# Performance work log

Measured on AMD Instinct MI355X. Metric: run time of the kernel, lower is better.

The kernel has to match this reference:

```python
import jax, jax.numpy as jnp
import numpy as np


def setup_inputs() -> dict:
    key = jax.random.key(0)
    k1, k2 = jax.random.split(key)
    N, M, D = 2048, 2048, 64
    z_x = jax.random.normal(k1, (N, D), dtype=jnp.float32)
    z_y = jax.random.normal(k2, (M, D), dtype=jnp.float32)
    return {"z_x": z_x, "z_y": z_y}


def reference(z_x, z_y):
    # s[i, j] = -sum_d |z_x[i, d] - z_y[j, d]|  -> [N, M]
    s = -jnp.sum(jnp.abs(z_x[:, None, :] - z_y[None, :, :]), axis=-1)
    a = jax.nn.softmax(s, axis=1)  # row softmax
    b = jax.nn.softmax(s, axis=0)  # column softmax
    w = a + b - a * b              # soft-or combination of alignments
    c = jnp.sum(w * s) / jnp.sum(w)
    return c
```

## Files before the change

kernel.cpp:

```cpp
#include <hip/hip_runtime.h>

#define NROWS 2048
#define MCOLS 2048
#define DDIM  64
#define TILE  64
#define NTI   32
#define NTJ   32

__device__ __forceinline__ void stage_tiles(
    const float* __restrict__ zx, const float* __restrict__ zy,
    int bi, int bj, float (*sX)[TILE], float (*sY)[TILE])
{
  int t = threadIdx.x;
  int r  = t & 63;
  int d0 = (t >> 6) << 2;
  const float* zxp = zx + (size_t)(bi * TILE + r) * DDIM;
  const float* zyp = zy + (size_t)(bj * TILE + r) * DDIM;
#pragma unroll
  for (int q = 0; q < 4; ++q) {
    int d = d0 + 16 * q;
    float4 xv = *(const float4*)(zxp + d);
    float4 yv = *(const float4*)(zyp + d);
    sX[d+0][r]=xv.x; sX[d+1][r]=xv.y; sX[d+2][r]=xv.z; sX[d+3][r]=xv.w;
    sY[d+0][r]=yv.x; sY[d+1][r]=yv.y; sY[d+2][r]=yv.z; sY[d+3][r]=yv.w;
  }
}

__device__ __forceinline__ void compute_sv(
    const float (*sX)[TILE], const float (*sY)[TILE],
    int i0, int j0, float sv[4][4])
{
  float acc[4][4] = {{0.f}};
#pragma unroll 8
  for (int d = 0; d < DDIM; ++d) {
    float4 xv = *(const float4*)&sX[d][i0];
    float4 yv = *(const float4*)&sY[d][j0];
    float xr[4] = {xv.x, xv.y, xv.z, xv.w};
    float yc[4] = {yv.x, yv.y, yv.z, yv.w};
#pragma unroll
    for (int a = 0; a < 4; ++a)
#pragma unroll
      for (int b = 0; b < 4; ++b)
        acc[a][b] += fabsf(xr[a] - yc[b]);
  }
#pragma unroll
  for (int a = 0; a < 4; ++a)
#pragma unroll
    for (int b = 0; b < 4; ++b)
      sv[a][b] = -acc[a][b];
}

__global__ __launch_bounds__(256) void k1_dist(
    const float* __restrict__ zx, const float* __restrict__ zy,
    float* __restrict__ s_out,
    float* __restrict__ rm_part, float* __restrict__ rs_part,
    float* __restrict__ cm_part, float* __restrict__ cs_part)
{
  __shared__ float sX[DDIM][TILE];
  __shared__ float sY[DDIM][TILE];
  __shared__ float cmw[4][TILE];
  __shared__ float csw[4][TILE];

  int bi = blockIdx.y, bj = blockIdx.x;
  int t  = threadIdx.x;
  int lid = t & 63, wv = t >> 6;
  int i0 = (t >> 4) << 2, j0 = (t & 15) << 2;

  stage_tiles(zx, zy, bi, bj, sX, sY);
  __syncthreads();
  float sv[4][4];
  compute_sv(sX, sY, i0, j0, sv);

#pragma unroll
  for (int a = 0; a < 4; ++a) {
    float4 v = make_float4(sv[a][0], sv[a][1], sv[a][2], sv[a][3]);
    *(float4*)(s_out + (size_t)(bi * TILE + i0 + a) * MCOLS + bj * TILE + j0) = v;
  }

  float rm[4], es[4];
#pragma unroll
  for (int a = 0; a < 4; ++a)
    rm[a] = fmaxf(fmaxf(sv[a][0], sv[a][1]), fmaxf(sv[a][2], sv[a][3]));
#pragma unroll
  for (int off = 1; off <= 8; off <<= 1)
#pragma unroll
    for (int a = 0; a < 4; ++a)
      rm[a] = fmaxf(rm[a], __shfl_xor(rm[a], off));
#pragma unroll
  for (int a = 0; a < 4; ++a)
    es[a] = __expf(sv[a][0]-rm[a]) + __expf(sv[a][1]-rm[a])
          + __expf(sv[a][2]-rm[a]) + __expf(sv[a][3]-rm[a]);
#pragma unroll
  for (int off = 1; off <= 8; off <<= 1)
#pragma unroll
    for (int a = 0; a < 4; ++a)
      es[a] += __shfl_xor(es[a], off);
  if ((lid & 15) == 0) {
#pragma unroll
    for (int a = 0; a < 4; ++a) {
      int idx = bj * NROWS + bi * TILE + i0 + a;
      rm_part[idx] = rm[a];
      rs_part[idx] = es[a];
    }
  }

  float cm[4], ce[4];
#pragma unroll
  for (int b = 0; b < 4; ++b)
    cm[b] = fmaxf(fmaxf(sv[0][b], sv[1][b]), fmaxf(sv[2][b], sv[3][b]));
#pragma unroll
  for (int off = 16; off <= 32; off <<= 1)
#pragma unroll
    for (int b = 0; b < 4; ++b)
      cm[b] = fmaxf(cm[b], __shfl_xor(cm[b], off));
#pragma unroll
  for (int b = 0; b < 4; ++b)
    ce[b] = __expf(sv[0][b]-cm[b]) + __expf(sv[1][b]-cm[b])
          + __expf(sv[2][b]-cm[b]) + __expf(sv[3][b]-cm[b]);
#pragma unroll
  for (int off = 16; off <= 32; off <<= 1)
#pragma unroll
    for (int b = 0; b < 4; ++b)
      ce[b] += __shfl_xor(ce[b], off);
  if (lid < 16) {
#pragma unroll
    for (int b = 0; b < 4; ++b) {
      cmw[wv][lid * 4 + b] = cm[b];
      csw[wv][lid * 4 + b] = ce[b];
    }
  }
  __syncthreads();
  if (t < TILE) {
    int j = t;
    float M = fmaxf(fmaxf(cmw[0][j], cmw[1][j]), fmaxf(cmw[2][j], cmw[3][j]));
    float S = __expf(cmw[0][j]-M)*csw[0][j] + __expf(cmw[1][j]-M)*csw[1][j]
            + __expf(cmw[2][j]-M)*csw[2][j] + __expf(cmw[3][j]-M)*csw[3][j];
    int idx = bi * MCOLS + bj * TILE + j;
    cm_part[idx] = M;
    cs_part[idx] = S;
  }
}

__global__ __launch_bounds__(256) void k2_combine(
    const float* __restrict__ s_in,
    const float* __restrict__ rm_part, const float* __restrict__ rs_part,
    const float* __restrict__ cm_part, const float* __restrict__ cs_part,
    float* __restrict__ part )
{
  __shared__ float l_rmax[TILE], l_rinv[TILE];
  __shared__ float l_cmax[TILE], l_cinv[TILE];
  __shared__ float red[8];

  int bi = blockIdx.y, bj = blockIdx.x;
  int t  = threadIdx.x;
  int lid = t & 63, wv = t >> 6;
  int i0 = (t >> 4) << 2, j0 = (t & 15) << 2;

  if (t < 64) {
    int i = bi * TILE + t;
    float m[NTJ];
#pragma unroll
    for (int tj = 0; tj < NTJ; ++tj) m[tj] = rm_part[tj * NROWS + i];
    float M = m[0];
#pragma unroll
    for (int tj = 1; tj < NTJ; ++tj) M = fmaxf(M, m[tj]);
    float S = 0.f;
#pragma unroll
    for (int tj = 0; tj < NTJ; ++tj)
      S += __expf(m[tj] - M) * rs_part[tj * NROWS + i];
    l_rmax[t] = M;
    l_rinv[t] = 1.f / S;
  } else if (t < 128) {
    int c = t - 64;
    int j = bj * TILE + c;
    float m[NTI];
#pragma unroll
    for (int ti = 0; ti < NTI; ++ti) m[ti] = cm_part[ti * MCOLS + j];
    float M = m[0];
#pragma unroll
    for (int ti = 1; ti < NTI; ++ti) M = fmaxf(M, m[ti]);
    float S = 0.f;
#pragma unroll
    for (int ti = 0; ti < NTI; ++ti)
      S += __expf(m[ti] - M) * cs_part[ti * MCOLS + j];
    l_cmax[c] = M;
    l_cinv[c] = 1.f / S;
  }
  __syncthreads();

  float sv[4][4];
  {
    const float* base = s_in + (size_t)(bi * TILE + i0) * MCOLS + bj * TILE + j0;
#pragma unroll
    for (int a = 0; a < 4; ++a) {
      float4 v = *(const float4*)(base + (size_t)a * MCOLS);
      sv[a][0] = v.x; sv[a][1] = v.y; sv[a][2] = v.z; sv[a][3] = v.w;
    }
  }
  float rm[4], rv[4], cm[4], cv[4];
#pragma unroll
  for (int a = 0; a < 4; ++a) {
    rm[a] = l_rmax[i0 + a];
    rv[a] = l_rinv[i0 + a];
  }
#pragma unroll
  for (int b = 0; b < 4; ++b) {
    cm[b] = l_cmax[j0 + b];
    cv[b] = l_cinv[j0 + b];
  }
  float pn = 0.f, pd = 0.f;
#pragma unroll
  for (int a = 0; a < 4; ++a)
#pragma unroll
    for (int b = 0; b < 4; ++b) {
      float av = __expf(sv[a][b] - rm[a]) * rv[a];
      float bv = __expf(sv[a][b] - cm[b]) * cv[b];
      float w  = av + bv - av * bv;
      pn += w * sv[a][b];
      pd += w;
    }
#pragma unroll
  for (int off = 1; off <= 32; off <<= 1) {
    pn += __shfl_xor(pn, off);
    pd += __shfl_xor(pd, off);
  }
  if (lid == 0) { red[wv * 2] = pn; red[wv * 2 + 1] = pd; }
  __syncthreads();
  if (t == 0) {
    int bid = bi * NTJ + bj;
    part[bid * 2 + 0] = red[0] + red[2] + red[4] + red[6];
    part[bid * 2 + 1] = red[1] + red[3] + red[5] + red[7];
  }
}

__global__ __launch_bounds__(256) void k3_out(
    const float* __restrict__ part, float* __restrict__ out)
{
  int t = threadIdx.x;
  float pn = 0.f, pd = 0.f;
#pragma unroll
  for (int k = t; k < NTI * NTJ; k += 256) {
    float2 v = *(const float2*)(part + k * 2);
    pn += v.x;
    pd += v.y;
  }
#pragma unroll
  for (int off = 1; off <= 32; off <<= 1) {
    pn += __shfl_xor(pn, off);
    pd += __shfl_xor(pd, off);
  }
  __shared__ float red[8];
  if ((t & 63) == 0) { red[(t >> 6) * 2] = pn; red[(t >> 6) * 2 + 1] = pd; }
  __syncthreads();
  if (t == 0) {
    float n = red[0] + red[2] + red[4] + red[6];
    float d = red[1] + red[3] + red[5] + red[7];
    out[0] = n / d;
  }
}

extern "C" void kernel_launch(void* const* d_in, const int* in_sizes, int n_in,
                              void* d_out, int out_size, void* d_ws, size_t ws_size,
                              hipStream_t stream)
{
  const float* zx = (const float*)d_in[0];
  const float* zy = (const float*)d_in[1];
  float* out = (float*)d_out;

  char* ws = (char*)d_ws;
  float* part    = (float*)(ws + 0);
  float* rm_part = (float*)(ws + (64  << 10));
  float* rs_part = (float*)(ws + (320 << 10));
  float* cm_part = (float*)(ws + (576 << 10));
  float* cs_part = (float*)(ws + (832 << 10));
  float* s_buf   = (float*)(ws + (1088 << 10));

  dim3 grid(NTJ, NTI), block(256);
  k1_dist   <<<grid, block, 0, stream>>>(zx, zy, s_buf,
                                         rm_part, rs_part, cm_part, cs_part);
  k2_combine<<<grid, block, 0, stream>>>(s_buf,
                                         rm_part, rs_part, cm_part, cs_part, part);
  k3_out    <<<dim3(1), block, 0, stream>>>(part, out);
}
```

Baseline: 35.71 us.

## Enlarge distance tile to 128x64 with 8x4 per-thread microtile and nontemporal S traffic

```diff
diff --git a/kernel.cpp b/kernel.cpp
--- a/kernel.cpp
+++ b/kernel.cpp
@@ -3,52 +3,14 @@
 #define NROWS 2048
 #define MCOLS 2048
 #define DDIM  64
-#define TILE  64
-#define NTI   32
-#define NTJ   32
-
-__device__ __forceinline__ void stage_tiles(
-    const float* __restrict__ zx, const float* __restrict__ zy,
-    int bi, int bj, float (*sX)[TILE], float (*sY)[TILE])
-{
-  int t = threadIdx.x;
-  int r  = t & 63;
-  int d0 = (t >> 6) << 2;
-  const float* zxp = zx + (size_t)(bi * TILE + r) * DDIM;
-  const float* zyp = zy + (size_t)(bj * TILE + r) * DDIM;
-#pragma unroll
-  for (int q = 0; q < 4; ++q) {
-    int d = d0 + 16 * q;
-    float4 xv = *(const float4*)(zxp + d);
-    float4 yv = *(const float4*)(zyp + d);
-    sX[d+0][r]=xv.x; sX[d+1][r]=xv.y; sX[d+2][r]=xv.z; sX[d+3][r]=xv.w;
-    sY[d+0][r]=yv.x; sY[d+1][r]=yv.y; sY[d+2][r]=yv.z; sY[d+3][r]=yv.w;
-  }
-}
-
-__device__ __forceinline__ void compute_sv(
-    const float (*sX)[TILE], const float (*sY)[TILE],
-    int i0, int j0, float sv[4][4])
-{
-  float acc[4][4] = {{0.f}};
-#pragma unroll 8
-  for (int d = 0; d < DDIM; ++d) {
-    float4 xv = *(const float4*)&sX[d][i0];
-    float4 yv = *(const float4*)&sY[d][j0];
-    float xr[4] = {xv.x, xv.y, xv.z, xv.w};
-    float yc[4] = {yv.x, yv.y, yv.z, yv.w};
-#pragma unroll
-    for (int a = 0; a < 4; ++a)
-#pragma unroll
-      for (int b = 0; b < 4; ++b)
-        acc[a][b] += fabsf(xr[a] - yc[b]);
-  }
-#pragma unroll
-  for (int a = 0; a < 4; ++a)
-#pragma unroll
-    for (int b = 0; b < 4; ++b)
-      sv[a][b] = -acc[a][b];
-}
+#define TI    128
+#define TJ    64
+#define NTI1  (NROWS / TI)
+#define NTJ   (MCOLS / TJ)
+#define TILE2 64
+#define NTI2  (NROWS / TILE2)
+
+typedef float f32x4 __attribute__((ext_vector_type(4)));
 
 __global__ __launch_bounds__(256) void k1_dist(
     const float* __restrict__ zx, const float* __restrict__ zy,
@@ -56,88 +18,139 @@
     float* __restrict__ rm_part, float* __restrict__ rs_part,
     float* __restrict__ cm_part, float* __restrict__ cs_part)
 {
-  __shared__ float sX[DDIM][TILE];
-  __shared__ float sY[DDIM][TILE];
-  __shared__ float cmw[4][TILE];
-  __shared__ float csw[4][TILE];
-
-  int bi = blockIdx.y, bj = blockIdx.x;
-  int t  = threadIdx.x;
-  int lid = t & 63, wv = t >> 6;
-  int i0 = (t >> 4) << 2, j0 = (t & 15) << 2;
-
-  stage_tiles(zx, zy, bi, bj, sX, sY);
-  __syncthreads();
-  float sv[4][4];
-  compute_sv(sX, sY, i0, j0, sv);
-
-#pragma unroll
-  for (int a = 0; a < 4; ++a) {
-    float4 v = make_float4(sv[a][0], sv[a][1], sv[a][2], sv[a][3]);
-    *(float4*)(s_out + (size_t)(bi * TILE + i0 + a) * MCOLS + bj * TILE + j0) = v;
-  }
-
-  float rm[4], es[4];
-#pragma unroll
-  for (int a = 0; a < 4; ++a)
-    rm[a] = fmaxf(fmaxf(sv[a][0], sv[a][1]), fmaxf(sv[a][2], sv[a][3]));
-#pragma unroll
-  for (int off = 1; off <= 8; off <<= 1)
-#pragma unroll
-    for (int a = 0; a < 4; ++a)
-      rm[a] = fmaxf(rm[a], __shfl_xor(rm[a], off));
-#pragma unroll
-  for (int a = 0; a < 4; ++a)
-    es[a] = __expf(sv[a][0]-rm[a]) + __expf(sv[a][1]-rm[a])
-          + __expf(sv[a][2]-rm[a]) + __expf(sv[a][3]-rm[a]);
-#pragma unroll
-  for (int off = 1; off <= 8; off <<= 1)
-#pragma unroll
-    for (int a = 0; a < 4; ++a)
-      es[a] += __shfl_xor(es[a], off);
-  if ((lid & 15) == 0) {
-#pragma unroll
-    for (int a = 0; a < 4; ++a) {
-      int idx = bj * NROWS + bi * TILE + i0 + a;
-      rm_part[idx] = rm[a];
-      rs_part[idx] = es[a];
-    }
-  }
-
-  float cm[4], ce[4];
-#pragma unroll
-  for (int b = 0; b < 4; ++b)
-    cm[b] = fmaxf(fmaxf(sv[0][b], sv[1][b]), fmaxf(sv[2][b], sv[3][b]));
-#pragma unroll
-  for (int off = 16; off <= 32; off <<= 1)
+  __shared__ float sX[DDIM][TI];
+  __shared__ float sY[DDIM][TJ];
+  __shared__ float cmw[4][TJ];
+  __shared__ float csw[4][TJ];
+
+  const int bi = blockIdx.y, bj = blockIdx.x;
+  const int t  = threadIdx.x;
+  const int lid = t & 63, wv = t >> 6;
+  const int i0 = (t >> 4) << 3;
+  const int j0 = (t & 15) << 2;
+
+  {
+    int r = t & 127, half = t >> 7;
+    const float* zxp = zx + (size_t)(bi * TI + r) * DDIM + half * 32;
+#pragma unroll
+    for (int q = 0; q < 8; ++q) {
+      float4 v = *(const float4*)(zxp + q * 4);
+      int d = half * 32 + q * 4;
+      sX[d+0][r]=v.x; sX[d+1][r]=v.y; sX[d+2][r]=v.z; sX[d+3][r]=v.w;
+    }
+  }
+  {
+    int r = t & 63, quad = t >> 6;
+    const float* zyp = zy + (size_t)(bj * TJ + r) * DDIM + quad * 16;
+#pragma unroll
+    for (int q = 0; q < 4; ++q) {
+      float4 v = *(const float4*)(zyp + q * 4);
+      int d = quad * 16 + q * 4;
+      sY[d+0][r]=v.x; sY[d+1][r]=v.y; sY[d+2][r]=v.z; sY[d+3][r]=v.w;
+    }
+  }
+  __syncthreads();
+
+  float acc[8][4] = {{0.f}};
+#pragma unroll 4
+  for (int d = 0; d < DDIM; ++d) {
+    float4 x0 = *(const float4*)&sX[d][i0];
+    float4 x1 = *(const float4*)&sX[d][i0 + 4];
+    float4 yv = *(const float4*)&sY[d][j0];
+    float xr[8] = {x0.x, x0.y, x0.z, x0.w, x1.x, x1.y, x1.z, x1.w};
+    float yc[4] = {yv.x, yv.y, yv.z, yv.w};
+#pragma unroll
+    for (int a = 0; a < 8; ++a)
+#pragma unroll
+      for (int b = 0; b < 4; ++b)
+        acc[a][b] += fabsf(xr[a] - yc[b]);
+  }
+  float sv[8][4];
+#pragma unroll
+  for (int a = 0; a < 8; ++a)
 #pragma unroll
     for (int b = 0; b < 4; ++b)
-      cm[b] = fmaxf(cm[b], __shfl_xor(cm[b], off));
-#pragma unroll
-  for (int b = 0; b < 4; ++b)
-    ce[b] = __expf(sv[0][b]-cm[b]) + __expf(sv[1][b]-cm[b])
-          + __expf(sv[2][b]-cm[b]) + __expf(sv[3][b]-cm[b]);
-#pragma unroll
-  for (int off = 16; off <= 32; off <<= 1)
-#pragma unroll
-    for (int b = 0; b < 4; ++b)
-      ce[b] += __shfl_xor(ce[b], off);
-  if (lid < 16) {
+      sv[a][b] = -acc[a][b];
+
+#pragma unroll
+  for (int a = 0; a < 8; ++a) {
+    f32x4 v = { sv[a][0], sv[a][1], sv[a][2], sv[a][3] };
+    __builtin_nontemporal_store(v,
+        (f32x4*)(s_out + (size_t)(bi * TI + i0 + a) * MCOLS + bj * TJ + j0));
+  }
+
+  {
+    float rm[8], es[8];
+#pragma unroll
+    for (int a = 0; a < 8; ++a)
+      rm[a] = fmaxf(fmaxf(sv[a][0], sv[a][1]), fmaxf(sv[a][2], sv[a][3]));
+#pragma unroll
+    for (int off = 1; off <= 8; off <<= 1)
+#pragma unroll
+      for (int a = 0; a < 8; ++a)
+        rm[a] = fmaxf(rm[a], __shfl_xor(rm[a], off));
+#pragma unroll
+    for (int a = 0; a < 8; ++a)
+      es[a] = __expf(sv[a][0]-rm[a]) + __expf(sv[a][1]-rm[a])
+            + __expf(sv[a][2]-rm[a]) + __expf(sv[a][3]-rm[a]);
+#pragma unroll
+    for (int off = 1; off <= 8; off <<= 1)
+#pragma unroll
+      for (int a = 0; a < 8; ++a)
+        es[a] += __shfl_xor(es[a], off);
+    if ((lid & 15) == 0) {
+#pragma unroll
+      for (int a = 0; a < 8; ++a) {
+        int idx = bj * NROWS + bi * TI + i0 + a;
+        rm_part[idx] = rm[a];
+        rs_part[idx] = es[a];
+      }
+    }
+  }
+
+  {
+    float cm[4], ce[4];
 #pragma unroll
     for (int b = 0; b < 4; ++b) {
-      cmw[wv][lid * 4 + b] = cm[b];
-      csw[wv][lid * 4 + b] = ce[b];
-    }
-  }
-  __syncthreads();
-  if (t < TILE) {
-    int j = t;
-    float M = fmaxf(fmaxf(cmw[0][j], cmw[1][j]), fmaxf(cmw[2][j], cmw[3][j]));
-    float S = __expf(cmw[0][j]-M)*csw[0][j] + __expf(cmw[1][j]-M)*csw[1][j]
-            + __expf(cmw[2][j]-M)*csw[2][j] + __expf(cmw[3][j]-M)*csw[3][j];
-    int idx = bi * MCOLS + bj * TILE + j;
-    cm_part[idx] = M;
-    cs_part[idx] = S;
+      float m = sv[0][b];
+#pragma unroll
+      for (int a = 1; a < 8; ++a) m = fmaxf(m, sv[a][b]);
+      cm[b] = m;
+    }
+#pragma unroll
+    for (int off = 16; off <= 32; off <<= 1)
+#pragma unroll
+      for (int b = 0; b < 4; ++b)
+        cm[b] = fmaxf(cm[b], __shfl_xor(cm[b], off));
+#pragma unroll
+    for (int b = 0; b < 4; ++b) {
+      float s = 0.f;
+#pragma unroll
+      for (int a = 0; a < 8; ++a) s += __expf(sv[a][b] - cm[b]);
+      ce[b] = s;
+    }
+#pragma unroll
+    for (int off = 16; off <= 32; off <<= 1)
+#pragma unroll
+      for (int b = 0; b < 4; ++b)
+        ce[b] += __shfl_xor(ce[b], off);
+    if (lid < 16) {
+#pragma unroll
+      for (int b = 0; b < 4; ++b) {
+        cmw[wv][lid * 4 + b] = cm[b];
+        csw[wv][lid * 4 + b] = ce[b];
+      }
+    }
+    __syncthreads();
+    if (t < TJ) {
+      int j = t;
+      float M = fmaxf(fmaxf(cmw[0][j], cmw[1][j]), fmaxf(cmw[2][j], cmw[3][j]));
+      float S = __expf(cmw[0][j]-M)*csw[0][j] + __expf(cmw[1][j]-M)*csw[1][j]
+              + __expf(cmw[2][j]-M)*csw[2][j] + __expf(cmw[3][j]-M)*csw[3][j];
+      int idx = bi * MCOLS + bj * TJ + j;
+      cm_part[idx] = M;
+      cs_part[idx] = S;
+    }
   }
 }
 
@@ -147,8 +160,8 @@
     const float* __restrict__ cm_part, const float* __restrict__ cs_part,
     float* __restrict__ part )
 {
-  __shared__ float l_rmax[TILE], l_rinv[TILE];
-  __shared__ float l_cmax[TILE], l_cinv[TILE];
+  __shared__ float l_rmax[TILE2], l_rinv[TILE2];
+  __shared__ float l_cmax[TILE2], l_cinv[TILE2];
   __shared__ float red[8];
 
   int bi = blockIdx.y, bj = blockIdx.x;
@@ -157,7 +170,7 @@
   int i0 = (t >> 4) << 2, j0 = (t & 15) << 2;
 
   if (t < 64) {
-    int i = bi * TILE + t;
+    int i = bi * TILE2 + t;
     float m[NTJ];
 #pragma unroll
     for (int tj = 0; tj < NTJ; ++tj) m[tj] = rm_part[tj * NROWS + i];
@@ -172,16 +185,16 @@
     l_rinv[t] = 1.f / S;
   } else if (t < 128) {
     int c = t - 64;
-    int j = bj * TILE + c;
-    float m[NTI];
-#pragma unroll
-    for (int ti = 0; ti < NTI; ++ti) m[ti] = cm_part[ti * MCOLS + j];
+    int j = bj * TILE2 + c;
+    float m[NTI1];
+#pragma unroll
+    for (int ti = 0; ti < NTI1; ++ti) m[ti] = cm_part[ti * MCOLS + j];
     float M = m[0];
 #pragma unroll
-    for (int ti = 1; ti < NTI; ++ti) M = fmaxf(M, m[ti]);
+    for (int ti = 1; ti < NTI1; ++ti) M = fmaxf(M, m[ti]);
     float S = 0.f;
 #pragma unroll
-    for (int ti = 0; ti < NTI; ++ti)
+    for (int ti = 0; ti < NTI1; ++ti)
       S += __expf(m[ti] - M) * cs_part[ti * MCOLS + j];
     l_cmax[c] = M;
     l_cinv[c] = 1.f / S;
@@ -190,10 +203,11 @@
 
   float sv[4][4];
   {
-    const float* base = s_in + (size_t)(bi * TILE + i0) * MCOLS + bj * TILE + j0;
+    const float* base = s_in + (size_t)(bi * TILE2 + i0) * MCOLS + bj * TILE2 + j0;
 #pragma unroll
     for (int a = 0; a < 4; ++a) {
-      float4 v = *(const float4*)(base + (size_t)a * MCOLS);
+      f32x4 v = __builtin_nontemporal_load(
+          (const f32x4*)(base + (size_t)a * MCOLS));
       sv[a][0] = v.x; sv[a][1] = v.y; sv[a][2] = v.z; sv[a][3] = v.w;
     }
   }
@@ -239,7 +253,7 @@
   int t = threadIdx.x;
   float pn = 0.f, pd = 0.f;
 #pragma unroll
-  for (int k = t; k < NTI * NTJ; k += 256) {
+  for (int k = t; k < NTI2 * NTJ; k += 256) {
     float2 v = *(const float2*)(part + k * 2);
     pn += v.x;
     pd += v.y;
@@ -275,10 +289,9 @@
   float* cs_part = (float*)(ws + (832 << 10));
   float* s_buf   = (float*)(ws + (1088 << 10));
 
-  dim3 grid(NTJ, NTI), block(256);
-  k1_dist   <<<grid, block, 0, stream>>>(zx, zy, s_buf,
-                                         rm_part, rs_part, cm_part, cs_part);
-  k2_combine<<<grid, block, 0, stream>>>(s_buf,
-                                         rm_part, rs_part, cm_part, cs_part, part);
-  k3_out    <<<dim3(1), block, 0, stream>>>(part, out);
-}
+  k1_dist   <<<dim3(NTJ, NTI1), dim3(256), 0, stream>>>(zx, zy, s_buf,
+                rm_part, rs_part, cm_part, cs_part);
+  k2_combine<<<dim3(NTJ, NTI2), dim3(256), 0, stream>>>(s_buf,
+                rm_part, rs_part, cm_part, cs_part, part);
+  k3_out    <<<dim3(1), dim3(256), 0, stream>>>(part, out);
+}
```

Result: slower. 36.66 us (+2.6%).

## Store distance matrix in fp16 and fuse final reduction via last-block ticket

Applied to the files above, without the earlier changes.

```diff
diff --git a/kernel.cpp b/kernel.cpp
--- a/kernel.cpp
+++ b/kernel.cpp
@@ -1,4 +1,5 @@
 #include <hip/hip_runtime.h>
+#include <hip/hip_fp16.h>
 
 #define NROWS 2048
 #define MCOLS 2048
@@ -6,30 +7,41 @@
 #define TILE  64
 #define NTI   32
 #define NTJ   32
-
-__device__ __forceinline__ void stage_tiles(
+#define NBLK2 (NTI * NTJ)
+
+__global__ __launch_bounds__(256) void k1_dist(
     const float* __restrict__ zx, const float* __restrict__ zy,
-    int bi, int bj, float (*sX)[TILE], float (*sY)[TILE])
+    __half* __restrict__ s_out,
+    float* __restrict__ rm_part, float* __restrict__ rs_part,
+    float* __restrict__ cm_part, float* __restrict__ cs_part)
 {
-  int t = threadIdx.x;
-  int r  = t & 63;
-  int d0 = (t >> 6) << 2;
-  const float* zxp = zx + (size_t)(bi * TILE + r) * DDIM;
-  const float* zyp = zy + (size_t)(bj * TILE + r) * DDIM;
-#pragma unroll
-  for (int q = 0; q < 4; ++q) {
-    int d = d0 + 16 * q;
-    float4 xv = *(const float4*)(zxp + d);
-    float4 yv = *(const float4*)(zyp + d);
-    sX[d+0][r]=xv.x; sX[d+1][r]=xv.y; sX[d+2][r]=xv.z; sX[d+3][r]=xv.w;
-    sY[d+0][r]=yv.x; sY[d+1][r]=yv.y; sY[d+2][r]=yv.z; sY[d+3][r]=yv.w;
-  }
-}
-
-__device__ __forceinline__ void compute_sv(
-    const float (*sX)[TILE], const float (*sY)[TILE],
-    int i0, int j0, float sv[4][4])
-{
+  __shared__ float sX[DDIM][TILE];
+  __shared__ float sY[DDIM][TILE];
+  __shared__ float cmw[4][TILE];
+  __shared__ float csw[4][TILE];
+
+  const int bi = blockIdx.y, bj = blockIdx.x;
+  const int t  = threadIdx.x;
+  const int lid = t & 63, wv = t >> 6;
+  const int i0 = (t >> 4) << 2;
+  const int j0 = (t & 15) << 2;
+
+  {
+    int r  = t & 63;
+    int d0 = (t >> 6) << 2;
+    const float* zxp = zx + (size_t)(bi * TILE + r) * DDIM;
+    const float* zyp = zy + (size_t)(bj * TILE + r) * DDIM;
+#pragma unroll
+    for (int q = 0; q < 4; ++q) {
+      int d = d0 + 16 * q;
+      float4 xv = *(const float4*)(zxp + d);
+      float4 yv = *(const float4*)(zyp + d);
+      sX[d+0][r]=xv.x; sX[d+1][r]=xv.y; sX[d+2][r]=xv.z; sX[d+3][r]=xv.w;
+      sY[d+0][r]=yv.x; sY[d+1][r]=yv.y; sY[d+2][r]=yv.z; sY[d+3][r]=yv.w;
+    }
+  }
+  __syncthreads();
+
   float acc[4][4] = {{0.f}};
 #pragma unroll 8
   for (int d = 0; d < DDIM; ++d) {
@@ -43,113 +55,100 @@
       for (int b = 0; b < 4; ++b)
         acc[a][b] += fabsf(xr[a] - yc[b]);
   }
-#pragma unroll
-  for (int a = 0; a < 4; ++a)
+
+  float sv[4][4];
+#pragma unroll
+  for (int a = 0; a < 4; ++a) {
+    __half2 h01 = __floats2half2_rn(-acc[a][0], -acc[a][1]);
+    __half2 h23 = __floats2half2_rn(-acc[a][2], -acc[a][3]);
+    uint2 u;
+    u.x = *(const unsigned*)&h01;
+    u.y = *(const unsigned*)&h23;
+    *(uint2*)(s_out + (size_t)(bi * TILE + i0 + a) * MCOLS + bj * TILE + j0) = u;
+    float2 f01 = __half22float2(h01), f23 = __half22float2(h23);
+    sv[a][0] = f01.x; sv[a][1] = f01.y; sv[a][2] = f23.x; sv[a][3] = f23.y;
+  }
+
+  {
+    float rm[4], es[4];
+#pragma unroll
+    for (int a = 0; a < 4; ++a)
+      rm[a] = fmaxf(fmaxf(sv[a][0], sv[a][1]), fmaxf(sv[a][2], sv[a][3]));
+#pragma unroll
+    for (int off = 1; off <= 8; off <<= 1)
+#pragma unroll
+      for (int a = 0; a < 4; ++a)
+        rm[a] = fmaxf(rm[a], __shfl_xor(rm[a], off));
+#pragma unroll
+    for (int a = 0; a < 4; ++a)
+      es[a] = __expf(sv[a][0]-rm[a]) + __expf(sv[a][1]-rm[a])
+            + __expf(sv[a][2]-rm[a]) + __expf(sv[a][3]-rm[a]);
+#pragma unroll
+    for (int off = 1; off <= 8; off <<= 1)
+#pragma unroll
+      for (int a = 0; a < 4; ++a)
+        es[a] += __shfl_xor(es[a], off);
+    if ((lid & 15) == 0) {
+#pragma unroll
+      for (int a = 0; a < 4; ++a) {
+        int idx = bj * NROWS + bi * TILE + i0 + a;
+        rm_part[idx] = rm[a];
+        rs_part[idx] = es[a];
+      }
+    }
+  }
+
+  {
+    float cm[4], ce[4];
 #pragma unroll
     for (int b = 0; b < 4; ++b)
-      sv[a][b] = -acc[a][b];
+      cm[b] = fmaxf(fmaxf(sv[0][b], sv[1][b]), fmaxf(sv[2][b], sv[3][b]));
+#pragma unroll
+    for (int off = 16; off <= 32; off <<= 1)
+#pragma unroll
+      for (int b = 0; b < 4; ++b)
+        cm[b] = fmaxf(cm[b], __shfl_xor(cm[b], off));
+#pragma unroll
+    for (int b = 0; b < 4; ++b)
+      ce[b] = __expf(sv[0][b]-cm[b]) + __expf(sv[1][b]-cm[b])
+            + __expf(sv[2][b]-cm[b]) + __expf(sv[3][b]-cm[b]);
+#pragma unroll
+    for (int off = 16; off <= 32; off <<= 1)
+#pragma unroll
+      for (int b = 0; b < 4; ++b)
+        ce[b] += __shfl_xor(ce[b], off);
+    if (lid < 16) {
+#pragma unroll
+      for (int b = 0; b < 4; ++b) {
+        cmw[wv][lid * 4 + b] = cm[b];
+        csw[wv][lid * 4 + b] = ce[b];
+      }
+    }
+    __syncthreads();
+    if (t < TILE) {
+      int j = t;
+      float M = fmaxf(fmaxf(cmw[0][j], cmw[1][j]), fmaxf(cmw[2][j], cmw[3][j]));
+      float S = __expf(cmw[0][j]-M)*csw[0][j] + __expf(cmw[1][j]-M)*csw[1][j]
+              + __expf(cmw[2][j]-M)*csw[2][j] + __expf(cmw[3][j]-M)*csw[3][j];
+      int idx = bi * MCOLS + bj * TILE + j;
+      cm_part[idx] = M;
+      cs_part[idx] = S;
+    }
+  }
 }
 
-__global__ __launch_bounds__(256) void k1_dist(
-    const float* __restrict__ zx, const float* __restrict__ zy,
-    float* __restrict__ s_out,
-    float* __restrict__ rm_part, float* __restrict__ rs_part,
-    float* __restrict__ cm_part, float* __restrict__ cs_part)
-{
-  __shared__ float sX[DDIM][TILE];
-  __shared__ float sY[DDIM][TILE];
-  __shared__ float cmw[4][TILE];
-  __shared__ float csw[4][TILE];
-
-  int bi = blockIdx.y, bj = blockIdx.x;
-  int t  = threadIdx.x;
-  int lid = t & 63, wv = t >> 6;
-  int i0 = (t >> 4) << 2, j0 = (t & 15) << 2;
-
-  stage_tiles(zx, zy, bi, bj, sX, sY);
-  __syncthreads();
-  float sv[4][4];
-  compute_sv(sX, sY, i0, j0, sv);
-
-#pragma unroll
-  for (int a = 0; a < 4; ++a) {
-    float4 v = make_float4(sv[a][0], sv[a][1], sv[a][2], sv[a][3]);
-    *(float4*)(s_out + (size_t)(bi * TILE + i0 + a) * MCOLS + bj * TILE + j0) = v;
-  }
-
-  float rm[4], es[4];
-#pragma unroll
-  for (int a = 0; a < 4; ++a)
-    rm[a] = fmaxf(fmaxf(sv[a][0], sv[a][1]), fmaxf(sv[a][2], sv[a][3]));
-#pragma unroll
-  for (int off = 1; off <= 8; off <<= 1)
-#pragma unroll
-    for (int a = 0; a < 4; ++a)
-      rm[a] = fmaxf(rm[a], __shfl_xor(rm[a], off));
-#pragma unroll
-  for (int a = 0; a < 4; ++a)
-    es[a] = __expf(sv[a][0]-rm[a]) + __expf(sv[a][1]-rm[a])
-          + __expf(sv[a][2]-rm[a]) + __expf(sv[a][3]-rm[a]);
-#pragma unroll
-  for (int off = 1; off <= 8; off <<= 1)
-#pragma unroll
-    for (int a = 0; a < 4; ++a)
-      es[a] += __shfl_xor(es[a], off);
-  if ((lid & 15) == 0) {
-#pragma unroll
-    for (int a = 0; a < 4; ++a) {
-      int idx = bj * NROWS + bi * TILE + i0 + a;
-      rm_part[idx] = rm[a];
-      rs_part[idx] = es[a];
-    }
-  }
-
-  float cm[4], ce[4];
-#pragma unroll
-  for (int b = 0; b < 4; ++b)
-    cm[b] = fmaxf(fmaxf(sv[0][b], sv[1][b]), fmaxf(sv[2][b], sv[3][b]));
-#pragma unroll
-  for (int off = 16; off <= 32; off <<= 1)
-#pragma unroll
-    for (int b = 0; b < 4; ++b)
-      cm[b] = fmaxf(cm[b], __shfl_xor(cm[b], off));
-#pragma unroll
-  for (int b = 0; b < 4; ++b)
-    ce[b] = __expf(sv[0][b]-cm[b]) + __expf(sv[1][b]-cm[b])
-          + __expf(sv[2][b]-cm[b]) + __expf(sv[3][b]-cm[b]);
-#pragma unroll
-  for (int off = 16; off <= 32; off <<= 1)
-#pragma unroll
-    for (int b = 0; b < 4; ++b)
-      ce[b] += __shfl_xor(ce[b], off);
-  if (lid < 16) {
-#pragma unroll
-    for (int b = 0; b < 4; ++b) {
-      cmw[wv][lid * 4 + b] = cm[b];
-      csw[wv][lid * 4 + b] = ce[b];
-    }
-  }
-  __syncthreads();
-  if (t < TILE) {
-    int j = t;
-    float M = fmaxf(fmaxf(cmw[0][j], cmw[1][j]), fmaxf(cmw[2][j], cmw[3][j]));
-    float S = __expf(cmw[0][j]-M)*csw[0][j] + __expf(cmw[1][j]-M)*csw[1][j]
-            + __expf(cmw[2][j]-M)*csw[2][j] + __expf(cmw[3][j]-M)*csw[3][j];
-    int idx = bi * MCOLS + bj * TILE + j;
-    cm_part[idx] = M;
-    cs_part[idx] = S;
-  }
-}
-
 __global__ __launch_bounds__(256) void k2_combine(
-    const float* __restrict__ s_in,
+    const __half* __restrict__ s_in,
     const float* __restrict__ rm_part, const float* __restrict__ rs_part,
     const float* __restrict__ cm_part, const float* __restrict__ cs_part,
-    float* __restrict__ part )
+    float* __restrict__ part ,
+    unsigned* __restrict__ ticket,
+    float* __restrict__ out)
 {
   __shared__ float l_rmax[TILE], l_rinv[TILE];
   __shared__ float l_cmax[TILE], l_cinv[TILE];
   __shared__ float red[8];
+  __shared__ int winner;
 
   int bi = blockIdx.y, bj = blockIdx.x;
   int t  = threadIdx.x;
@@ -190,11 +189,14 @@
 
   float sv[4][4];
   {
-    const float* base = s_in + (size_t)(bi * TILE + i0) * MCOLS + bj * TILE + j0;
+    const __half* base = s_in + (size_t)(bi * TILE + i0) * MCOLS + bj * TILE + j0;
 #pragma unroll
     for (int a = 0; a < 4; ++a) {
-      float4 v = *(const float4*)(base + (size_t)a * MCOLS);
-      sv[a][0] = v.x; sv[a][1] = v.y; sv[a][2] = v.z; sv[a][3] = v.w;
+      uint2 u = *(const uint2*)(base + (size_t)a * MCOLS);
+      __half2 h01 = *(const __half2*)&u.x;
+      __half2 h23 = *(const __half2*)&u.y;
+      float2 f01 = __half22float2(h01), f23 = __half22float2(h23);
+      sv[a][0] = f01.x; sv[a][1] = f01.y; sv[a][2] = f23.x; sv[a][3] = f23.y;
     }
   }
   float rm[4], rv[4], cm[4], cv[4];
@@ -228,34 +230,41 @@
   __syncthreads();
   if (t == 0) {
     int bid = bi * NTJ + bj;
-    part[bid * 2 + 0] = red[0] + red[2] + red[4] + red[6];
-    part[bid * 2 + 1] = red[1] + red[3] + red[5] + red[7];
-  }
-}
-
-__global__ __launch_bounds__(256) void k3_out(
-    const float* __restrict__ part, float* __restrict__ out)
-{
-  int t = threadIdx.x;
-  float pn = 0.f, pd = 0.f;
-#pragma unroll
-  for (int k = t; k < NTI * NTJ; k += 256) {
-    float2 v = *(const float2*)(part + k * 2);
-    pn += v.x;
-    pd += v.y;
-  }
-#pragma unroll
-  for (int off = 1; off <= 32; off <<= 1) {
-    pn += __shfl_xor(pn, off);
-    pd += __shfl_xor(pd, off);
-  }
-  __shared__ float red[8];
-  if ((t & 63) == 0) { red[(t >> 6) * 2] = pn; red[(t >> 6) * 2 + 1] = pd; }
-  __syncthreads();
-  if (t == 0) {
-    float n = red[0] + red[2] + red[4] + red[6];
-    float d = red[1] + red[3] + red[5] + red[7];
-    out[0] = n / d;
+    float2 p;
+    p.x = red[0] + red[2] + red[4] + red[6];
+    p.y = red[1] + red[3] + red[5] + red[7];
+    *(float2*)(part + bid * 2) = p;
+    __threadfence();
+    unsigned old = __hip_atomic_fetch_add(ticket, 1u, __ATOMIC_ACQ_REL,
+                                          __HIP_MEMORY_SCOPE_AGENT);
+    winner = (old == NBLK2 - 1);
+  }
+  __syncthreads();
+
+  if (winner) {
+    float qn = 0.f, qd = 0.f;
+#pragma unroll
+    for (int k = t; k < NBLK2; k += 256) {
+      unsigned long long uv = __hip_atomic_load(
+          (const unsigned long long*)(part + k * 2),
+          __ATOMIC_RELAXED, __HIP_MEMORY_SCOPE_AGENT);
+      union { unsigned long long u; float2 f; } cvt;
+      cvt.u = uv;
+      qn += cvt.f.x;
+      qd += cvt.f.y;
+    }
+#pragma unroll
+    for (int off = 1; off <= 32; off <<= 1) {
+      qn += __shfl_xor(qn, off);
+      qd += __shfl_xor(qd, off);
+    }
+    if (lid == 0) { red[wv * 2] = qn; red[wv * 2 + 1] = qd; }
+    __syncthreads();
+    if (t == 0) {
+      float n = red[0] + red[2] + red[4] + red[6];
+      float d = red[1] + red[3] + red[5] + red[7];
+      out[0] = n / d;
+    }
   }
 }
 
@@ -268,17 +277,19 @@
   float* out = (float*)d_out;
 
   char* ws = (char*)d_ws;
-  float* part    = (float*)(ws + 0);
+  unsigned* ticket = (unsigned*)(ws + 0);
+  float* part    = (float*)(ws + (8  << 10));
   float* rm_part = (float*)(ws + (64  << 10));
   float* rs_part = (float*)(ws + (320 << 10));
   float* cm_part = (float*)(ws + (576 << 10));
   float* cs_part = (float*)(ws + (832 << 10));
-  float* s_buf   = (float*)(ws + (1088 << 10));
+  __half* s_buf  = (__half*)(ws + (1088 << 10));
+
+  hipMemsetAsync(ticket, 0, 64, stream);
 
   dim3 grid(NTJ, NTI), block(256);
   k1_dist   <<<grid, block, 0, stream>>>(zx, zy, s_buf,
-                                         rm_part, rs_part, cm_part, cs_part);
+                rm_part, rs_part, cm_part, cs_part);
   k2_combine<<<grid, block, 0, stream>>>(s_buf,
-                                         rm_part, rs_part, cm_part, cs_part, part);
-  k3_out    <<<dim3(1), block, 0, stream>>>(part, out);
+                rm_part, rs_part, cm_part, cs_part, part, ticket, out);
 }
```

After: 67.55 us. 89.1% more time.
